# Kernel optimization log

Measured on AMD Instinct MI355X. Metric: run time of the kernel, lower is better.

The kernel has to match this reference:

```python
import jax, jax.numpy as jnp
import numpy as np

N = 4096

def setup_inputs() -> dict:
    key = jax.random.key(0)
    kA, kB = jax.random.split(key)
    # A and B are upper-triangular inputs, as the module assumes
    A = jnp.triu(jax.random.normal(kA, (N, N), dtype=jnp.float32))
    B = jnp.triu(jax.random.normal(kB, (N, N), dtype=jnp.float32))
    return {"A": A, "B": B}

def reference(A, B):
    # C = triu(A @ B); product of upper-triangular matrices is upper-triangular,
    # the kernel additionally masks the lower triangle of the output.
    return jnp.triu(A @ B)
```

## Files before the change

### kernel.cpp

```cpp
#include <hip/hip_runtime.h>


#define N   4096
#define NB  32
#define BM  128
#define BK  32
#define CH  8
#define NWG 1000

typedef __attribute__((ext_vector_type(8))) __bf16 bf16x8;
typedef __attribute__((ext_vector_type(4))) float  floatx4;
typedef __attribute__((ext_vector_type(8))) unsigned short ushort8;

__device__ __forceinline__ unsigned short f32_to_bf16_rne(float f) {
    unsigned u = __builtin_bit_cast(unsigned, f);
    unsigned r = u + 0x7fffu + ((u >> 16) & 1u);
    return (unsigned short)(r >> 16);
}

__global__ __launch_bounds__(256)
void prep_kernel(const float* __restrict__ A, const float* __restrict__ B,
                 unsigned short* __restrict__ Ab, unsigned short* __restrict__ Bt,
                 float* __restrict__ C) {
    __shared__ float tile[64][65];
    const int bx = blockIdx.x, by = blockIdx.y;
    const int x0 = bx * 64, y0 = by * 64;
    const int xb = bx >> 1, yb = by >> 1;
    const int t  = threadIdx.x;
    const int tr = t >> 2, tc = (t & 3) * 16;

    if (xb >= yb) {
        const float* src = A + (size_t)(y0 + tr) * N + x0 + tc;
        const float4 v0 = ((const float4*)src)[0];
        const float4 v1 = ((const float4*)src)[1];
        const float4 v2 = ((const float4*)src)[2];
        const float4 v3 = ((const float4*)src)[3];
        ushort8 o0, o1;
        o0[0]=f32_to_bf16_rne(v0.x); o0[1]=f32_to_bf16_rne(v0.y);
        o0[2]=f32_to_bf16_rne(v0.z); o0[3]=f32_to_bf16_rne(v0.w);
        o0[4]=f32_to_bf16_rne(v1.x); o0[5]=f32_to_bf16_rne(v1.y);
        o0[6]=f32_to_bf16_rne(v1.z); o0[7]=f32_to_bf16_rne(v1.w);
        o1[0]=f32_to_bf16_rne(v2.x); o1[1]=f32_to_bf16_rne(v2.y);
        o1[2]=f32_to_bf16_rne(v2.z); o1[3]=f32_to_bf16_rne(v2.w);
        o1[4]=f32_to_bf16_rne(v3.x); o1[5]=f32_to_bf16_rne(v3.y);
        o1[6]=f32_to_bf16_rne(v3.z); o1[7]=f32_to_bf16_rne(v3.w);
        unsigned short* dst = Ab + (size_t)(y0 + tr) * N + x0 + tc;
        ((ushort8*)dst)[0] = o0;
        ((ushort8*)dst)[1] = o1;
    }
    if (xb <= yb) {
        const float* src = B + (size_t)(x0 + tr) * N + y0 + tc;
        const float4 v0 = ((const float4*)src)[0];
        const float4 v1 = ((const float4*)src)[1];
        const float4 v2 = ((const float4*)src)[2];
        const float4 v3 = ((const float4*)src)[3];
        float* d = &tile[tr][tc];
        d[0]=v0.x; d[1]=v0.y; d[2]=v0.z; d[3]=v0.w;
        d[4]=v1.x; d[5]=v1.y; d[6]=v1.z; d[7]=v1.w;
        d[8]=v2.x; d[9]=v2.y; d[10]=v2.z; d[11]=v2.w;
        d[12]=v3.x; d[13]=v3.y; d[14]=v3.z; d[15]=v3.w;
        __syncthreads();
        ushort8 o0, o1;
        #pragma unroll
        for (int i = 0; i < 8; ++i) o0[i] = f32_to_bf16_rne(tile[tc + i][tr]);
        #pragma unroll
        for (int i = 0; i < 8; ++i) o1[i] = f32_to_bf16_rne(tile[tc + 8 + i][tr]);
        unsigned short* dst = Bt + (size_t)(y0 + tr) * N + x0 + tc;
        ((ushort8*)dst)[0] = o0;
        ((ushort8*)dst)[1] = o1;
    }
    if (xb < yb || (xb - yb) >= CH) {
        float4 z = {0.f, 0.f, 0.f, 0.f};
        float* dst = C + (size_t)(y0 + tr) * N + x0 + tc;
        ((float4*)dst)[0] = z; ((float4*)dst)[1] = z;
        ((float4*)dst)[2] = z; ((float4*)dst)[3] = z;
    }
}

__global__ __launch_bounds__(256)
void trimm_kernel(const unsigned short* __restrict__ Ab,
                  const unsigned short* __restrict__ Bt,
                  float* __restrict__ C) {
    __shared__ unsigned short sA[2][BM * BK];
    __shared__ unsigned short sB[2][BM * BK];

    int rem = blockIdx.x;
    int d = 0, per = 1;
    for (int dd = NB - 1; dd >= 0; --dd) {
        const int p   = (dd + CH) / CH;
        const int cnt = (NB - dd) * p;
        if (rem < cnt) { d = dd; per = p; break; }
        rem -= cnt;
    }
    const int tile  = rem / per;
    const int chunk = rem - tile * per;
    const int bi = tile, bj = tile + d;
    const int c    = d + 1;
    const int base = c / per, extra = c - base * per;
    const int kb0  = bi + chunk * base + (chunk < extra ? chunk : extra);
    const int len  = base + (chunk < extra ? 1 : 0);

    const int tid  = threadIdx.x;
    const int w    = tid >> 6;
    const int lane = tid & 63;
    const int quad = lane >> 4;
    const int l15  = lane & 15;

    const int m0 = (w >> 1) * 64;
    const int n0 = (w & 1) * 64;
    const int row0 = bi * BM;
    const int col0 = bj * BM;

    floatx4 acc[4][4] = {};

    const int srow = lane >> 2;
    const int skk  = (lane & 3) * 8;
    const int q0 = w * 2, q1 = w * 2 + 1;
    const int r0 = q0 * 16 + srow, r1 = q1 * 16 + srow;
    const int lofs0 = q0 * 512 + srow * 32 + skk;
    const int lofs1 = q1 * 512 + srow * 32 + skk;

    const unsigned short* gA0 = Ab + (size_t)(row0 + r0) * N + kb0 * BM + skk;
    const unsigned short* gA1 = Ab + (size_t)(row0 + r1) * N + kb0 * BM + skk;
    const unsigned short* gB0 = Bt + (size_t)(col0 + r0) * N + kb0 * BM + skk;
    const unsigned short* gB1 = Bt + (size_t)(col0 + r1) * N + kb0 * BM + skk;

    const int ns = len * 4;

    ushort8 aR0 = *(const ushort8*)gA0;  gA0 += BK;
    ushort8 aR1 = *(const ushort8*)gA1;  gA1 += BK;
    ushort8 bR0 = *(const ushort8*)gB0;  gB0 += BK;
    ushort8 bR1 = *(const ushort8*)gB1;  gB1 += BK;

    for (int s = 0; s < ns; ++s) {
        const int buf = s & 1;
        *(ushort8*)&sA[buf][lofs0] = aR0;
        *(ushort8*)&sA[buf][lofs1] = aR1;
        *(ushort8*)&sB[buf][lofs0] = bR0;
        *(ushort8*)&sB[buf][lofs1] = bR1;
        __syncthreads();
        if (s + 1 < ns) {
            aR0 = *(const ushort8*)gA0;  gA0 += BK;
            aR1 = *(const ushort8*)gA1;  gA1 += BK;
            bR0 = *(const ushort8*)gB0;  gB0 += BK;
            bR1 = *(const ushort8*)gB1;  gB1 += BK;
        }
        bf16x8 af[4], bfr[4];
        #pragma unroll
        for (int t = 0; t < 4; ++t) {
            af[t]  = *(const bf16x8*)&sA[buf][(m0 + t * 16 + l15) * BK + quad * 8];
            bfr[t] = *(const bf16x8*)&sB[buf][(n0 + t * 16 + l15) * BK + quad * 8];
        }
        #pragma unroll
        for (int tm = 0; tm < 4; ++tm)
            #pragma unroll
            for (int tn = 0; tn < 4; ++tn)
                acc[tm][tn] = __builtin_amdgcn_mfma_f32_16x16x32_bf16(
                    af[tm], bfr[tn], acc[tm][tn], 0, 0, 0);
    }

    #pragma unroll
    for (int tm = 0; tm < 4; ++tm) {
        const int grow_base = row0 + m0 + tm * 16 + quad * 4;
        #pragma unroll
        for (int tn = 0; tn < 4; ++tn) {
            const int gcol = col0 + n0 + tn * 16 + l15;
            #pragma unroll
            for (int r = 0; r < 4; ++r) {
                const int grow = grow_base + r;
                float* p = C + (size_t)grow * N + gcol;
                const float v = acc[tm][tn][r];
                if (per > 1) {
                    atomicAdd(p, v);
                } else if (d != 0) {
                    *p = v;
                } else {
                    *p = (gcol >= grow) ? v : 0.0f;
                }
            }
        }
    }
}

extern "C" void kernel_launch(void* const* d_in, const int* in_sizes, int n_in,
                              void* d_out, int out_size, void* d_ws, size_t ws_size,
                              hipStream_t stream) {
    const float* A = (const float*)d_in[0];
    const float* B = (const float*)d_in[1];
    float* C = (float*)d_out;

    unsigned short* Ab = (unsigned short*)d_ws;
    unsigned short* Bt = Ab + (size_t)N * N;

    prep_kernel<<<dim3(N / 64, N / 64), dim3(256), 0, stream>>>(A, B, Ab, Bt, C);
    trimm_kernel<<<dim3(NWG), dim3(256), 0, stream>>>(Ab, Bt, C);
}
```

Baseline: 243.0 us.

## Double K-step per barrier with padded LDS rows and two-wave occupancy hint

Each pipeline phase of the triangular GEMM now stages a 64-wide K slab instead of 32, which halves the number of barriers and raises the number of MFMAs per sync. LDS rows are padded to a stride of 72 to reduce bank conflicts on the fragment reads. The kernel also requests two workgroups per CU through launch_bounds, and the last phase is peeled so no loads are issued past the end. The cost is more LDS use (about 72KB per block) and more prefetch registers, which may limit the occupancy the hint asks for.

New measurement: 234.7 us. 1.04x faster.

```diff
diff --git a/kernel.cpp b/kernel.cpp
--- a/kernel.cpp
+++ b/kernel.cpp
@@ -4,9 +4,10 @@
 #define N   4096
 #define NB  32
 #define BM  128
-#define BK  32
+#define PK  64
 #define CH  8
 #define NWG 1000
+#define RS  72
 
 typedef __attribute__((ext_vector_type(8))) __bf16 bf16x8;
 typedef __attribute__((ext_vector_type(4))) float  floatx4;
@@ -77,12 +78,12 @@
     }
 }
 
-__global__ __launch_bounds__(256)
+__global__ __launch_bounds__(256, 2)
 void trimm_kernel(const unsigned short* __restrict__ Ab,
                   const unsigned short* __restrict__ Bt,
                   float* __restrict__ C) {
-    __shared__ unsigned short sA[2][BM * BK];
-    __shared__ unsigned short sB[2][BM * BK];
+    __shared__ unsigned short sA[2][BM * RS];
+    __shared__ unsigned short sB[2][BM * RS];
 
     int rem = blockIdx.x;
     int d = 0, per = 1;
@@ -113,50 +114,66 @@
 
     floatx4 acc[4][4] = {};
 
-    const int srow = lane >> 2;
-    const int skk  = (lane & 3) * 8;
-    const int q0 = w * 2, q1 = w * 2 + 1;
-    const int r0 = q0 * 16 + srow, r1 = q1 * 16 + srow;
-    const int lofs0 = q0 * 512 + srow * 32 + skk;
-    const int lofs1 = q1 * 512 + srow * 32 + skk;
-
-    const unsigned short* gA0 = Ab + (size_t)(row0 + r0) * N + kb0 * BM + skk;
-    const unsigned short* gA1 = Ab + (size_t)(row0 + r1) * N + kb0 * BM + skk;
-    const unsigned short* gB0 = Bt + (size_t)(col0 + r0) * N + kb0 * BM + skk;
-    const unsigned short* gB1 = Bt + (size_t)(col0 + r1) * N + kb0 * BM + skk;
-
-    const int ns = len * 4;
-
-    ushort8 aR0 = *(const ushort8*)gA0;  gA0 += BK;
-    ushort8 aR1 = *(const ushort8*)gA1;  gA1 += BK;
-    ushort8 bR0 = *(const ushort8*)gB0;  gB0 += BK;
-    ushort8 bR1 = *(const ushort8*)gB1;  gB1 += BK;
-
-    for (int s = 0; s < ns; ++s) {
-        const int buf = s & 1;
-        *(ushort8*)&sA[buf][lofs0] = aR0;
-        *(ushort8*)&sA[buf][lofs1] = aR1;
-        *(ushort8*)&sB[buf][lofs0] = bR0;
-        *(ushort8*)&sB[buf][lofs1] = bR1;
+    const int srow8 = lane >> 3;
+    const int sk    = (lane & 7) * 8;
+    int lofs[4];
+    const unsigned short* gA[4];
+    const unsigned short* gB[4];
+    #pragma unroll
+    for (int i = 0; i < 4; ++i) {
+        const int r = w * 32 + i * 8 + srow8;
+        lofs[i] = r * RS + sk;
+        gA[i] = Ab + (size_t)(row0 + r) * N + kb0 * BM + sk;
+        gB[i] = Bt + (size_t)(col0 + r) * N + kb0 * BM + sk;
+    }
+
+    const int np = len * 2;
+
+    ushort8 aR[4], bR[4];
+    #pragma unroll
+    for (int i = 0; i < 4; ++i) { aR[i] = *(const ushort8*)gA[i]; gA[i] += PK; }
+    #pragma unroll
+    for (int i = 0; i < 4; ++i) { bR[i] = *(const ushort8*)gB[i]; gB[i] += PK; }
+
+    auto compute_phase = [&](int buf) {
+        #pragma unroll
+        for (int h = 0; h < 2; ++h) {
+            bf16x8 af[4], bfr[4];
+            #pragma unroll
+            for (int t = 0; t < 4; ++t) {
+                af[t]  = *(const bf16x8*)&sA[buf][(m0 + t * 16 + l15) * RS + h * 32 + quad * 8];
+                bfr[t] = *(const bf16x8*)&sB[buf][(n0 + t * 16 + l15) * RS + h * 32 + quad * 8];
+            }
+            #pragma unroll
+            for (int tm = 0; tm < 4; ++tm)
+                #pragma unroll
+                for (int tn = 0; tn < 4; ++tn)
+                    acc[tm][tn] = __builtin_amdgcn_mfma_f32_16x16x32_bf16(
+                        af[tm], bfr[tn], acc[tm][tn], 0, 0, 0);
+        }
+    };
+
+    for (int p = 0; p < np - 1; ++p) {
+        const int buf = p & 1;
+        #pragma unroll
+        for (int i = 0; i < 4; ++i) *(ushort8*)&sA[buf][lofs[i]] = aR[i];
+        #pragma unroll
+        for (int i = 0; i < 4; ++i) *(ushort8*)&sB[buf][lofs[i]] = bR[i];
         __syncthreads();
-        if (s + 1 < ns) {
-            aR0 = *(const ushort8*)gA0;  gA0 += BK;
-            aR1 = *(const ushort8*)gA1;  gA1 += BK;
-            bR0 = *(const ushort8*)gB0;  gB0 += BK;
-            bR1 = *(const ushort8*)gB1;  gB1 += BK;
-        }
-        bf16x8 af[4], bfr[4];
-        #pragma unroll
-        for (int t = 0; t < 4; ++t) {
-            af[t]  = *(const bf16x8*)&sA[buf][(m0 + t * 16 + l15) * BK + quad * 8];
-            bfr[t] = *(const bf16x8*)&sB[buf][(n0 + t * 16 + l15) * BK + quad * 8];
-        }
-        #pragma unroll
-        for (int tm = 0; tm < 4; ++tm)
-            #pragma unroll
-            for (int tn = 0; tn < 4; ++tn)
-                acc[tm][tn] = __builtin_amdgcn_mfma_f32_16x16x32_bf16(
-                    af[tm], bfr[tn], acc[tm][tn], 0, 0, 0);
+        #pragma unroll
+        for (int i = 0; i < 4; ++i) { aR[i] = *(const ushort8*)gA[i]; gA[i] += PK; }
+        #pragma unroll
+        for (int i = 0; i < 4; ++i) { bR[i] = *(const ushort8*)gB[i]; gB[i] += PK; }
+        compute_phase(buf);
+    }
+    {
+        const int buf = (np - 1) & 1;
+        #pragma unroll
+        for (int i = 0; i < 4; ++i) *(ushort8*)&sA[buf][lofs[i]] = aR[i];
+        #pragma unroll
+        for (int i = 0; i < 4; ++i) *(ushort8*)&sB[buf][lofs[i]] = bR[i];
+        __syncthreads();
+        compute_phase(buf);
     }
 
     #pragma unroll
```
